# Kernel optimization log

Hardware: AMD Instinct MI355X
Metric: run time of the kernel (lower is better)

The kernel has to match this reference:

```python
import jax, jax.numpy as jnp
import numpy as np
from itertools import product

L0 = (41, 1600, 1408)  # sparse_shape (z,y,x) from pc_range / voxel_size + [1,0,0]
B = 4
N_PER = 25000
PNAMES = ['w_in','s_in','b_in','w1','s1','b1','w2a','s2a','b2a','w2b','s2b','b2b','w2c','s2c','b2c','w3a','s3a','b3a','w3b','s3b','b3b','w3c','s3c','b3c','w4a','s4a','b4a','w4b','s4b','b4b','w4c','s4c','b4c','w_out','s_out','b_out']


def _enc(c, shape):
    D, H, W = shape
    return ((c[:, 0].astype(np.int64) * D + c[:, 1]) * H + c[:, 2]) * W + c[:, 3]


def _subm_rb(coords, shape):
    # submanifold conv rulebook: out site i gathers input j with coord_j = coord_i + offset
    N = coords.shape[0]
    keys = _enc(coords, shape)
    order = np.argsort(keys); sk = keys[order]
    ins, outs = [], []
    for dz, dy, dx in product((-1, 0, 1), repeat=3):
        nb = coords.astype(np.int64).copy()
        nb[:, 1] += dz; nb[:, 2] += dy; nb[:, 3] += dx
        ok = ((nb[:, 1] >= 0) & (nb[:, 1] < shape[0]) & (nb[:, 2] >= 0) & (nb[:, 2] < shape[1]) & (nb[:, 3] >= 0) & (nb[:, 3] < shape[2]))
        qi = np.nonzero(ok)[0]
        qk = _enc(nb[qi], shape)
        pos = np.clip(np.searchsorted(sk, qk), 0, N - 1)
        f = sk[pos] == qk
        ins.append(order[pos[f]].astype(np.int32))
        outs.append(qi[f].astype(np.int32))
    R = max(len(a) for a in ins)
    rin = np.zeros((27, R), np.int32); rout = np.full((27, R), N, np.int32)  # pad -> dummy out row
    for k in range(27):
        rin[k, :len(ins[k])] = ins[k]; rout[k, :len(outs[k])] = outs[k]
    return jnp.asarray(rin), jnp.asarray(rout)


def _spconv_rb(coords, shape, ks, st, pd):
    # strided sparse conv: out = (in + pad - k) / stride where divisible and in-bounds
    osh = tuple((shape[i] + 2 * pd[i] - ks[i]) // st[i] + 1 for i in range(3))
    per = []; allk = []
    for off in product(*[range(k) for k in ks]):
        oc = np.empty((coords.shape[0], 4), np.int64)
        oc[:, 0] = coords[:, 0]
        ok = np.ones(coords.shape[0], bool)
        for d in range(3):
            v = coords[:, d + 1].astype(np.int64) + pd[d] - off[d]
            ok &= (v % st[d] == 0)
            v = v // st[d]
            ok &= (v >= 0) & (v < osh[d])
            oc[:, d + 1] = v
        qi = np.nonzero(ok)[0]
        qk = _enc(oc[qi], osh)
        per.append((qi.astype(np.int32), qk)); allk.append(qk)
    uk = np.unique(np.concatenate(allk))
    Nout = len(uk); K = len(per)
    R = max(len(qi) for qi, _ in per)
    rin = np.zeros((K, R), np.int32); rout = np.full((K, R), Nout, np.int32)
    for k, (qi, qk) in enumerate(per):
        rin[k, :len(qi)] = qi
        rout[k, :len(qi)] = np.searchsorted(uk, qk).astype(np.int32)
    t = uk.copy()
    x = t % osh[2]; t //= osh[2]; y = t % osh[1]; t //= osh[1]; z = t % osh[0]; b = t // osh[0]
    ocoords = np.stack([b, z, y, x], 1).astype(np.int32)
    return jnp.asarray(rin), jnp.asarray(rout), ocoords, osh


def _gen_coords(rng):
    # clustered LiDAR-like voxel occupancy: gaussian clusters so 3x3x3 neighborhoods are populated
    out = []
    for b in range(B):
        nc = 250
        ctr = np.stack([rng.integers(6, 34, nc), rng.integers(60, 1540, nc), rng.integers(60, 1348, nc)], 1)
        pts = ctr[np.repeat(np.arange(nc), 400)] + rng.normal(0.0, 2.0, (nc * 400, 3))
        pts = np.rint(pts).astype(np.int64)
        for d in range(3):
            pts[:, d] = np.clip(pts[:, d], 0, L0[d] - 1)
        keys = (pts[:, 0] * L0[1] + pts[:, 1]) * L0[2] + pts[:, 2]
        _, ui = np.unique(keys, return_index=True)
        assert len(ui) >= N_PER
        c = pts[np.sort(ui[:N_PER])]
        out.append(np.concatenate([np.full((N_PER, 1), b, np.int64), c], 1))
    return np.concatenate(out, 0).astype(np.int32)


def _conv(feat, W, rin, rout, nout):
    # gather -> per-offset GEMM -> scatter-add (spconv rulebook algorithm)
    out = jnp.zeros((nout + 1, W.shape[2]), feat.dtype)  # +1 dummy row for padding
    for k in range(W.shape[0]):
        out = out.at[rout[k]].add(feat[rin[k]] @ W[k])
    return out[:nout]


def _bnrelu(x, s, b):
    # eval-mode BatchNorm1d folded to affine, then ReLU
    return jax.nn.relu(x * s + b)


def _net(voxels, normalizer, rb1_in, rb1_out, rb2s_in, rb2s_out, batch2, rb2_in, rb2_out, rb3s_in, rb3s_out, batch3, rb3_in, rb3_out, rb4s_in, rb4s_out, batch4, rb4_in, rb4_out, rbo_in, rbo_out, batch_out, P):
    n0 = voxels.shape[0]; n2 = batch2.shape[0]; n3 = batch3.shape[0]; n4 = batch4.shape[0]; no = batch_out.shape[0]
    f = voxels.sum(1) / normalizer  # mean VFE: (N0, 4)
    x = _bnrelu(_conv(f, P['w_in'], rb1_in, rb1_out, n0), P['s_in'], P['b_in'])
    x = _bnrelu(_conv(x, P['w1'], rb1_in, rb1_out, n0), P['s1'], P['b1'])
    x = _bnrelu(_conv(x, P['w2a'], rb2s_in, rb2s_out, n2), P['s2a'], P['b2a'])
    x = _bnrelu(_conv(x, P['w2b'], rb2_in, rb2_out, n2), P['s2b'], P['b2b'])
    x = _bnrelu(_conv(x, P['w2c'], rb2_in, rb2_out, n2), P['s2c'], P['b2c'])
    x = _bnrelu(_conv(x, P['w3a'], rb3s_in, rb3s_out, n3), P['s3a'], P['b3a'])
    x = _bnrelu(_conv(x, P['w3b'], rb3_in, rb3_out, n3), P['s3b'], P['b3b'])
    x = _bnrelu(_conv(x, P['w3c'], rb3_in, rb3_out, n3), P['s3c'], P['b3c'])
    x = _bnrelu(_conv(x, P['w4a'], rb4s_in, rb4s_out, n4), P['s4a'], P['b4a'])
    x = _bnrelu(_conv(x, P['w4b'], rb4_in, rb4_out, n4), P['s4b'], P['b4b'])
    x = _bnrelu(_conv(x, P['w4c'], rb4_in, rb4_out, n4), P['s4c'], P['b4c'])
    x = _bnrelu(_conv(x, P['w_out'], rbo_in, rbo_out, no), P['s_out'], P['b_out'])
    # per-batch global max pool over active voxels (== F.max_pool1d over voxel dim)
    return jax.ops.segment_max(x, batch_out.astype(jnp.int32), num_segments=B)


def setup_inputs():
    rng = np.random.default_rng(0)
    coords0 = _gen_coords(rng)
    rb1_in, rb1_out = _subm_rb(coords0, L0)
    rb2s_in, rb2s_out, c2, sh2 = _spconv_rb(coords0, L0, (3, 3, 3), (2, 2, 2), (1, 1, 1))
    rb2_in, rb2_out = _subm_rb(c2, sh2)
    rb3s_in, rb3s_out, c3, sh3 = _spconv_rb(c2, sh2, (3, 3, 3), (2, 2, 2), (1, 1, 1))
    rb3_in, rb3_out = _subm_rb(c3, sh3)
    rb4s_in, rb4s_out, c4, sh4 = _spconv_rb(c3, sh3, (3, 3, 3), (2, 2, 2), (0, 1, 1))
    rb4_in, rb4_out = _subm_rb(c4, sh4)
    rbo_in, rbo_out, co, _ = _spconv_rb(c4, sh4, (3, 1, 1), (2, 1, 1), (0, 0, 0))
    N0 = coords0.shape[0]
    d = dict(
        voxels=jnp.asarray(rng.normal(0, 1, (N0, 5, 4)).astype(np.float32)),
        voxel_num_points=jnp.asarray(rng.integers(1, 6, N0).astype(np.int32)),
        voxel_coords=jnp.asarray(coords0),
        rb1_in=rb1_in, rb1_out=rb1_out,
        rb2s_in=rb2s_in, rb2s_out=rb2s_out, batch2=jnp.asarray(c2[:, 0]),
        rb2_in=rb2_in, rb2_out=rb2_out,
        rb3s_in=rb3s_in, rb3s_out=rb3s_out, batch3=jnp.asarray(c3[:, 0]),
        rb3_in=rb3_in, rb3_out=rb3_out,
        rb4s_in=rb4s_in, rb4s_out=rb4s_out, batch4=jnp.asarray(c4[:, 0]),
        rb4_in=rb4_in, rb4_out=rb4_out,
        rbo_in=rbo_in, rbo_out=rbo_out, batch_out=jnp.asarray(co[:, 0]),
    )
    def _w(k, ci, co_):
        return jnp.asarray((rng.normal(0, 1, (k, ci, co_)) / np.sqrt(k * ci)).astype(np.float32))
    def _bn(c):
        return (jnp.asarray(rng.uniform(0.5, 1.5, c).astype(np.float32)), jnp.asarray(rng.normal(0, 0.1, c).astype(np.float32)))
    d['w_in'] = _w(27, 4, 16); d['s_in'], d['b_in'] = _bn(16)
    d['w1'] = _w(27, 16, 16); d['s1'], d['b1'] = _bn(16)
    d['w2a'] = _w(27, 16, 32); d['s2a'], d['b2a'] = _bn(32)
    d['w2b'] = _w(27, 32, 32); d['s2b'], d['b2b'] = _bn(32)
    d['w2c'] = _w(27, 32, 32); d['s2c'], d['b2c'] = _bn(32)
    d['w3a'] = _w(27, 32, 64); d['s3a'], d['b3a'] = _bn(64)
    d['w3b'] = _w(27, 64, 64); d['s3b'], d['b3b'] = _bn(64)
    d['w3c'] = _w(27, 64, 64); d['s3c'], d['b3c'] = _bn(64)
    d['w4a'] = _w(27, 64, 64); d['s4a'], d['b4a'] = _bn(64)
    d['w4b'] = _w(27, 64, 64); d['s4b'], d['b4b'] = _bn(64)
    d['w4c'] = _w(27, 64, 64); d['s4c'], d['b4c'] = _bn(64)
    d['w_out'] = _w(3, 64, 128); d['s_out'], d['b_out'] = _bn(128)
    return d


def reference(voxels, voxel_num_points, voxel_coords, rb1_in, rb1_out, rb2s_in, rb2s_out, batch2, rb2_in, rb2_out, rb3s_in, rb3s_out, batch3, rb3_in, rb3_out, rb4s_in, rb4s_out, batch4, rb4_in, rb4_out, rbo_in, rbo_out, batch_out, w_in, s_in, b_in, w1, s1, b1, w2a, s2a, b2a, w2b, s2b, b2b, w2c, s2c, b2c, w3a, s3a, b3a, w3b, s3b, b3b, w3c, s3c, b3c, w4a, s4a, b4a, w4b, s4b, b4b, w4c, s4c, b4c, w_out, s_out, b_out):
    normalizer = jnp.maximum(voxel_num_points.astype(voxels.dtype), 1.0)[:, None]
    P = dict(zip(PNAMES, (w_in, s_in, b_in, w1, s1, b1, w2a, s2a, b2a, w2b, s2b, b2b, w2c, s2c, b2c, w3a, s3a, b3a, w3b, s3b, b3b, w3c, s3c, b3c, w4a, s4a, b4a, w4b, s4b, b4b, w4c, s4c, b4c, w_out, s_out, b_out)))
    return _net(voxels, normalizer, rb1_in, rb1_out, rb2s_in, rb2s_out, batch2, rb2_in, rb2_out, rb3s_in, rb3s_out, batch3, rb3_in, rb3_out, rb4s_in, rb4s_out, batch4, rb4_in, rb4_out, rbo_in, rbo_out, batch_out, P)
```

## Files before the change

kernel.cpp:

```cpp
#include <hip/hip_runtime.h>
#include <cstddef>
#include <cstdint>

typedef _Float16 half8 __attribute__((ext_vector_type(8)));
typedef float floatx4 __attribute__((ext_vector_type(4)));
typedef float floatx16 __attribute__((ext_vector_type(16)));

static inline int cdiv_i(int a, int b) { return (a + b - 1) / b; }

struct RB { const int* rin; const int* rout; int K, R, nout, start, end, off; };
struct RBs { RB d[8]; };
__global__ void rb_fill_all(RBs P, int* __restrict__ tbl, int total) {
  int idx = blockIdx.x * blockDim.x + threadIdx.x;
  if (idx >= total) return;
#pragma unroll
  for (int l = 0; l < 8; ++l) {
    if (idx >= P.d[l].start && idx < P.d[l].end) {
      const RB rb = P.d[l];
      int e = idx - rb.start;
      int o = rb.rout[e];
      if ((unsigned)o < (unsigned)rb.nout) {
        int k = e / rb.R;
        tbl[rb.off + (size_t)k * rb.nout + o] = rb.rin[e];
      }
    }
  }
}

__global__ void tbl_fill_kernel(const int* __restrict__ rin,
                                const int* __restrict__ rout,
                                int* __restrict__ tbl, int K, int R, int nout) {
  int e = blockIdx.x * blockDim.x + threadIdx.x;
  if (e >= K * R) return;
  int o = rout[e];
  if ((unsigned)o >= (unsigned)nout) return;
  int k = e / R;
  tbl[(size_t)k * nout + o] = rin[e];
}

struct WP { const float* W; int K, Ci, CiPad, Co, start, end, off, p32; };
struct WPs {
  WP d[12];
  const float* vox; const int* vnp; _Float16* f0; int featTot, N0;
  float* dout; int outTot, wStart, wEnd;
};
__global__ void prep_all(WPs P, _Float16* __restrict__ Bp, int total) {
  int idx = blockIdx.x * blockDim.x + threadIdx.x;
  if (idx >= total) return;
  if (idx < P.featTot) {
    int i = idx >> 3, c = idx & 7;
    float v = 0.f;
    if (i < P.N0 && c < 4) {
      const float* p = P.vox + (size_t)i * 20 + c;
      v = (p[0] + p[4] + p[8] + p[12] + p[16]) / fmaxf((float)P.vnp[i], 1.f);
    }
    P.f0[idx] = (_Float16)v;
    return;
  }
  if (idx < P.featTot + P.outTot) {
    P.dout[idx - P.featTot] = 0.f;
    return;
  }
  int widx = idx - P.featTot - P.outTot;
#pragma unroll
  for (int l = 0; l < 12; ++l) {
    if (widx >= P.d[l].start && widx < P.d[l].end) {
      const WP w = P.d[l];
      int e = widx - w.start;
      int j = e & 7;
      int lane = (e >> 3) & 63;
      int rest = e >> 9;
      float v;
      if (w.p32) {
        int NT = w.Co >> 5;
        int t = rest % NT, ch = rest / NT;
        int SUB = w.CiPad >> 4;
        int ko = ch / SUB, s = ch % SUB;
        int ci = s * 16 + ((lane >> 5) << 3) + j;
        int col = t * 32 + (lane & 31);
        v = w.W[((size_t)ko * w.Ci + ci) * w.Co + col];
      } else {
        int NT = w.Co >> 4;
        int t = rest % NT, ch = rest / NT;
        int kk = ch * 32 + ((lane >> 4) << 3) + j;
        int k = kk / w.CiPad, ci = kk % w.CiPad;
        int n = t * 16 + (lane & 15);
        v = (k < w.K && ci < w.Ci) ? w.W[((size_t)k * w.Ci + ci) * w.Co + n] : 0.f;
      }
      Bp[w.off + e] = (_Float16)v;
    }
  }
}

template <int K, int CiPad, int Co, int KS, int CG, int CBLK>
__global__ __launch_bounds__(256) void conv_mfma(
    const _Float16* __restrict__ feat, const _Float16* __restrict__ Bp,
    const int* __restrict__ tbl, const float* __restrict__ sc,
    const float* __restrict__ bi, _Float16* __restrict__ out,
    int nout, int nin) {
  constexpr int NT = Co / 16;
  constexpr int NTE = NT / CBLK;
  constexpr int NTW = NTE / CG;
  constexpr int RG = 4 / (KS * CG);
  static_assert(KS * CG * RG == 4 && RG >= 1 && NT % CBLK == 0 && NTE % CG == 0);
  constexpr int NCH = (K * CiPad + 31) / 32;
  constexpr int L2C = (CiPad == 8) ? 3 : 4;
  constexpr int DIV = (CiPad >= 32) ? (CiPad / 32) : 1;
  constexpr int CoP = NTE * 16 + 4;

  __shared__ float red[(KS > 1) ? (KS - 1) * RG * 16 * CoP : 1];

  if (blockIdx.x == 0 && threadIdx.x < Co)
    out[(size_t)nout * Co + threadIdx.x] = (_Float16)0.f;

  int id = blockIdx.x;
  { int nb = gridDim.x, nb8 = (nb >> 3) << 3;
    if (id < nb8) { int per = nb >> 3; id = (id & 7) * per + (id >> 3); } }
  const int rt = id / CBLK, cb = id % CBLK;
  const int wave = threadIdx.x >> 6, lane = threadIdx.x & 63;
  const int ks = wave % KS;
  const int cg = (wave / KS) % CG;
  const int rowg = wave / (KS * CG);
  const int m = lane & 15, lb = (lane >> 4) * 8;
  const int i0 = (rt * RG + rowg) * 16;
  if constexpr (KS == 1) { if (i0 >= nout) return; }
  const int row = i0 + m;
  const bool rOK = row < nout;
  const int ct0 = cb * NTE + cg * NTW;

  floatx4 acc[NTW];
#pragma unroll
  for (int n = 0; n < NTW; ++n) { floatx4 z = {0,0,0,0}; acc[n] = z; }

  if constexpr (CiPad >= 32) {
    constexpr int NKW = (K + KS - 1) / KS;
    constexpr int NC = NKW * DIV;
    constexpr int DA = NC < 8 ? NC : 8;
    constexpr int DB = NC < 2 ? NC : 2;
    int idx[NKW];
#pragma unroll
    for (int q = 0; q < NKW; ++q) {
      int k = ks * NKW + q;
      int jj = (rOK && k < K) ? tbl[(size_t)k * nout + row] : -1;
      idx[q] = (jj < 0) ? nin : jj;
    }
    half8 ap[DA]; half8 bq[DB][NTW];
#pragma unroll
    for (int d = 0; d < DA; ++d)
      ap[d] = *(const half8*)(feat + (size_t)idx[d / DIV] * CiPad + (d % DIV) * 32 + lb);
#pragma unroll
    for (int d = 0; d < DB; ++d) {
      int k = ks * NKW + d / DIV;
      int ch = ((k < K) ? k : (K - 1)) * DIV + (d % DIV);
#pragma unroll
      for (int n = 0; n < NTW; ++n)
        bq[d][n] = *(const half8*)(Bp + ((size_t)ch * NT * 64 + lane) * 8 +
                                   (size_t)(ct0 + n) * 512);
    }
#pragma unroll
    for (int ii = 0; ii < NC; ++ii) {
      half8 a = ap[ii % DA];
      half8 bt[NTW];
#pragma unroll
      for (int n = 0; n < NTW; ++n) bt[n] = bq[ii % DB][n];
      if (ii + DA < NC) {
        int nx = ii + DA;
        ap[ii % DA] = *(const half8*)(feat + (size_t)idx[nx / DIV] * CiPad +
                                      (nx % DIV) * 32 + lb);
      }
      if (ii + DB < NC) {
        int nx = ii + DB;
        int k = ks * NKW + nx / DIV;
        int ch = ((k < K) ? k : (K - 1)) * DIV + (nx % DIV);
#pragma unroll
        for (int n = 0; n < NTW; ++n)
          bq[ii % DB][n] = *(const half8*)(Bp + ((size_t)ch * NT * 64 + lane) * 8 +
                                           (size_t)(ct0 + n) * 512);
      }
#pragma unroll
      for (int n = 0; n < NTW; ++n)
        acc[n] = __builtin_amdgcn_mfma_f32_16x16x32_f16(a, bt[n], acc[n], 0, 0, 0);
    }
  } else {
    constexpr int NCW = (NCH + KS - 1) / KS;
    constexpr int DA = NCW < 8 ? NCW : 8;
    constexpr int DB = NCW < 2 ? NCW : 2;
    int idx[NCW];
#pragma unroll
    for (int q = 0; q < NCW; ++q) {
      int ch = ks * NCW + q;
      int ko = (ch * 32 + lb) >> L2C;
      int jj = (rOK && ko < K && ch < NCH) ? tbl[(size_t)ko * nout + row] : -1;
      idx[q] = (jj < 0) ? nin : jj;
    }
    half8 ap[DA]; half8 bq[DB][NTW];
#pragma unroll
    for (int d = 0; d < DA; ++d) {
      int ch = ks * NCW + d;
      ap[d] = *(const half8*)(feat + (size_t)idx[d] * CiPad + ((ch * 32 + lb) & (CiPad - 1)));
    }
#pragma unroll
    for (int d = 0; d < DB; ++d) {
      int ch = ks * NCW + d;
      if (ch >= NCH) ch = NCH - 1;
#pragma unroll
      for (int n = 0; n < NTW; ++n)
        bq[d][n] = *(const half8*)(Bp + ((size_t)ch * NT * 64 + lane) * 8 +
                                   (size_t)(ct0 + n) * 512);
    }
#pragma unroll
    for (int ii = 0; ii < NCW; ++ii) {
      half8 a = ap[ii % DA];
      half8 bt[NTW];
#pragma unroll
      for (int n = 0; n < NTW; ++n) bt[n] = bq[ii % DB][n];
      if (ii + DA < NCW) {
        int nx = ii + DA;
        int ch = ks * NCW + nx;
        ap[ii % DA] = *(const half8*)(feat + (size_t)idx[nx] * CiPad +
                                      ((ch * 32 + lb) & (CiPad - 1)));
      }
      if (ii + DB < NCW) {
        int nx = ii + DB;
        int ch = ks * NCW + nx;
        if (ch >= NCH) ch = NCH - 1;
#pragma unroll
        for (int n = 0; n < NTW; ++n)
          bq[ii % DB][n] = *(const half8*)(Bp + ((size_t)ch * NT * 64 + lane) * 8 +
                                           (size_t)(ct0 + n) * 512);
      }
#pragma unroll
      for (int n = 0; n < NTW; ++n)
        acc[n] = __builtin_amdgcn_mfma_f32_16x16x32_f16(a, bt[n], acc[n], 0, 0, 0);
    }
  }

  const int rl = (lane >> 4) * 4;
  if constexpr (KS > 1) {
    if (ks > 0) {
#pragma unroll
      for (int n = 0; n < NTW; ++n) {
        int lcol = (cg * NTW + n) * 16 + m;
#pragma unroll
        for (int r = 0; r < 4; ++r)
          red[((ks - 1) * RG + rowg) * 16 * CoP + (rl + r) * CoP + lcol] = acc[n][r];
      }
    }
    __syncthreads();
    if (ks > 0) return;
#pragma unroll
    for (int s = 1; s < KS; ++s)
#pragma unroll
      for (int n = 0; n < NTW; ++n) {
        int lcol = (cg * NTW + n) * 16 + m;
#pragma unroll
        for (int r = 0; r < 4; ++r)
          acc[n][r] += red[((s - 1) * RG + rowg) * 16 * CoP + (rl + r) * CoP + lcol];
      }
  }

#pragma unroll
  for (int n = 0; n < NTW; ++n) {
    int col = (ct0 + n) * 16 + m;
    float s_ = sc[col], b_ = bi[col];
#pragma unroll
    for (int r = 0; r < 4; ++r) {
      int orow = i0 + rl + r;
      if (orow < nout)
        out[(size_t)orow * Co + col] = (_Float16)fmaxf(fmaf(acc[n][r], s_, b_), 0.f);
    }
  }
}

template <int K, int CiPad, int Co, int KS, int CG, int CBLK>
__global__ __launch_bounds__(256) void conv_mfma32(
    const _Float16* __restrict__ feat, const _Float16* __restrict__ Bp,
    const int* __restrict__ tbl, const float* __restrict__ sc,
    const float* __restrict__ bi, _Float16* __restrict__ out,
    int nout, int nin) {
  constexpr int NT = Co / 32;
  constexpr int NTE = NT / CBLK;
  constexpr int NTW = NTE / CG;
  constexpr int RG = 4 / (KS * CG);
  static_assert(KS * CG * RG == 4 && RG >= 1 && NT % CBLK == 0 && NTE % CG == 0 && NTW >= 1);
  constexpr int SUB = CiPad / 16;
  constexpr int NKW = (K + KS - 1) / KS;
  constexpr int NC = NKW * SUB;
  constexpr int DA = NC < 8 ? NC : 8;
  constexpr int DB = NC < 2 ? NC : 2;
  constexpr int CoP = NTE * 32 + 4;

  __shared__ float red[(KS > 1) ? (KS - 1) * RG * 32 * CoP : 1];

  if (blockIdx.x == 0 && threadIdx.x < Co)
    out[(size_t)nout * Co + threadIdx.x] = (_Float16)0.f;

  int id = blockIdx.x;
  { int nb = gridDim.x, nb8 = (nb >> 3) << 3;
    if (id < nb8) { int per = nb >> 3; id = (id & 7) * per + (id >> 3); } }
  const int rt = id / CBLK, cb = id % CBLK;
  const int wave = threadIdx.x >> 6, lane = threadIdx.x & 63;
  const int ks = wave % KS;
  const int cg = (wave / KS) % CG;
  const int rowg = wave / (KS * CG);
  const int m = lane & 31, lb = (lane >> 5) * 8, h = lane >> 5;
  const int i0 = (rt * RG + rowg) * 32;
  if constexpr (KS == 1) { if (i0 >= nout) return; }
  const int row = i0 + m;
  const bool rOK = row < nout;
  const int ct0 = cb * NTE + cg * NTW;

  floatx16 acc[NTW];
#pragma unroll
  for (int n = 0; n < NTW; ++n)
#pragma unroll
    for (int r = 0; r < 16; ++r) acc[n][r] = 0.f;

  int idx[NKW];
#pragma unroll
  for (int q = 0; q < NKW; ++q) {
    int k = ks * NKW + q;
    int jj = (rOK && k < K) ? tbl[(size_t)k * nout + row] : -1;
    idx[q] = (jj < 0) ? nin : jj;
  }

  half8 ap[DA]; half8 bq[DB][NTW];
#pragma unroll
  for (int d = 0; d < DA; ++d)
    ap[d] = *(const half8*)(feat + (size_t)idx[d / SUB] * CiPad + (d % SUB) * 16 + lb);
#pragma unroll
  for (int d = 0; d < DB; ++d) {
    int k = ks * NKW + d / SUB;
    int ch = ((k < K) ? k : (K - 1)) * SUB + (d % SUB);
#pragma unroll
    for (int n = 0; n < NTW; ++n)
      bq[d][n] = *(const half8*)(Bp + (size_t)(ch * NT + ct0 + n) * 512 + lane * 8);
  }
#pragma unroll
  for (int ii = 0; ii < NC; ++ii) {
    half8 a = ap[ii % DA];
    half8 bt[NTW];
#pragma unroll
    for (int n = 0; n < NTW; ++n) bt[n] = bq[ii % DB][n];
    if (ii + DA < NC) {
      int nx = ii + DA;
      ap[ii % DA] = *(const half8*)(feat + (size_t)idx[nx / SUB] * CiPad +
                                    (nx % SUB) * 16 + lb);
    }
    if (ii + DB < NC) {
      int nx = ii + DB;
      int k = ks * NKW + nx / SUB;
      int ch = ((k < K) ? k : (K - 1)) * SUB + (nx % SUB);
#pragma unroll
      for (int n = 0; n < NTW; ++n)
        bq[ii % DB][n] = *(const half8*)(Bp + (size_t)(ch * NT + ct0 + n) * 512 + lane * 8);
    }
#pragma unroll
    for (int n = 0; n < NTW; ++n)
      acc[n] = __builtin_amdgcn_mfma_f32_32x32x16_f16(a, bt[n], acc[n], 0, 0, 0);
  }

  if constexpr (KS > 1) {
    if (ks > 0) {
#pragma unroll
      for (int n = 0; n < NTW; ++n) {
        int lcol = (cg * NTW + n) * 32 + m;
#pragma unroll
        for (int reg = 0; reg < 16; ++reg) {
          int r = (reg & 3) + 8 * (reg >> 2) + 4 * h;
          red[((ks - 1) * RG + rowg) * 32 * CoP + r * CoP + lcol] = acc[n][reg];
        }
      }
    }
    __syncthreads();
    if (ks > 0) return;
#pragma unroll
    for (int s = 1; s < KS; ++s)
#pragma unroll
      for (int n = 0; n < NTW; ++n) {
        int lcol = (cg * NTW + n) * 32 + m;
#pragma unroll
        for (int reg = 0; reg < 16; ++reg) {
          int r = (reg & 3) + 8 * (reg >> 2) + 4 * h;
          acc[n][reg] += red[((s - 1) * RG + rowg) * 32 * CoP + r * CoP + lcol];
        }
      }
  }

#pragma unroll
  for (int n = 0; n < NTW; ++n) {
    int col = (ct0 + n) * 32 + m;
    float s_ = sc[col], b_ = bi[col];
#pragma unroll
    for (int reg = 0; reg < 16; ++reg) {
      int orow = i0 + (reg & 3) + 8 * (reg >> 2) + 4 * h;
      if (orow < nout)
        out[(size_t)orow * Co + col] = (_Float16)fmaxf(fmaf(acc[n][reg], s_, b_), 0.f);
    }
  }
}

__global__ __launch_bounds__(256) void segmax2(const _Float16* __restrict__ x,
                                               const int* __restrict__ batch,
                                               int n, float* __restrict__ out) {
  const int RPB = 128;
  int c = threadIdx.x & 127, g = threadIdx.x >> 7;
  int r0 = blockIdx.x * RPB + g;
  int rend = min(n, blockIdx.x * RPB + RPB);
  float mx = 0.f;
  int cb = -1;
  for (int r = r0; r < rend; r += 2) {
    int b = batch[r];
    if (b != cb) {
      if (cb >= 0) atomicMax((int*)out + ((size_t)cb << 7) + c, __float_as_int(mx));
      cb = b; mx = 0.f;
    }
    mx = fmaxf(mx, (float)x[(size_t)r * 128 + c]);
  }
  if (cb >= 0) atomicMax((int*)out + ((size_t)cb << 7) + c, __float_as_int(mx));
}

extern "C" void kernel_launch(void* const* d_in, const int* in_sizes, int n_in,
                              void* d_out, int out_size, void* d_ws, size_t ws_size,
                              hipStream_t stream) {
  auto I = [&](int idx) { return (const int*)d_in[idx]; };
  auto F = [&](int idx) { return (const float*)d_in[idx]; };

  const int N0  = in_sizes[1];
  const int R1  = in_sizes[3] / 27;
  const int R2s = in_sizes[5] / 27;
  const int n2  = in_sizes[7];
  const int R2  = in_sizes[8] / 27;
  const int R3s = in_sizes[10] / 27;
  const int n3  = in_sizes[12];
  const int R3  = in_sizes[13] / 27;
  const int R4s = in_sizes[15] / 27;
  const int n4  = in_sizes[17];
  const int R4  = in_sizes[18] / 27;
  const int Ro  = in_sizes[20] / 3;
  const int no  = in_sizes[22];

  const int wIdx[12] = {23, 26, 29, 32, 35, 38, 41, 44, 47, 50, 53, 56};
  const int Ks[12]   = {27, 27, 27, 27, 27, 27, 27, 27, 27, 27, 27, 3};
  const int Cis[12]  = {4, 16, 16, 32, 32, 32, 64, 64, 64, 64, 64, 64};
  const int Cos[12]  = {16, 16, 32, 32, 32, 64, 64, 64, 64, 64, 64, 128};
  const int P32[12]  = {0, 0, 0, 1, 1, 1, 1, 1, 1, 1, 1, 0};
  WPs P;
  int wtot = 0;
  int bpOff[12];
  for (int l = 0; l < 12; ++l) {
    int cip = Cis[l] < 8 ? 8 : Cis[l];
    int sz;
    if (P32[l]) sz = Ks[l] * (cip / 16) * (Cos[l] / 32) * 512;
    else        sz = ((Ks[l] * cip + 31) / 32) * (Cos[l] / 16) * 512;
    P.d[l].W = F(wIdx[l]);
    P.d[l].K = Ks[l]; P.d[l].Ci = Cis[l]; P.d[l].CiPad = cip; P.d[l].Co = Cos[l];
    P.d[l].start = wtot; P.d[l].end = wtot + sz; P.d[l].off = wtot; P.d[l].p32 = P32[l];
    bpOff[l] = wtot;
    wtot += sz;
  }

  RBs RP;
  const int rbRin[8]  = {3, 5, 8, 10, 13, 15, 18, 20};
  const int rbRs[8]   = {R1, R2s, R2, R3s, R3, R4s, R4, Ro};
  const int rbKs[8]   = {27, 27, 27, 27, 27, 27, 27, 3};
  const int rbNout[8] = {N0, n2, n2, n3, n3, n4, n4, no};
  size_t tblInts[8], tblOff[8];
  size_t totTbl = 0;
  int totFill = 0;
  for (int l = 0; l < 8; ++l) {
    tblInts[l] = (size_t)rbNout[l] * rbKs[l];
    tblOff[l] = totTbl;
    totTbl += tblInts[l];
    RP.d[l].rin = I(rbRin[l]);
    RP.d[l].rout = I(rbRin[l] + 1);
    RP.d[l].K = rbKs[l]; RP.d[l].R = rbRs[l]; RP.d[l].nout = rbNout[l];
    RP.d[l].start = totFill;
    totFill += rbKs[l] * rbRs[l];
    RP.d[l].end = totFill;
    RP.d[l].off = (int)tblOff[l];
  }

  size_t S = (size_t)(N0 + 1) * 16;
  auto smax = [&](size_t v) { if (v > S) S = v; };
  smax((size_t)(n2 + 1) * 32);
  smax((size_t)(n3 + 1) * 64);
  smax((size_t)(n4 + 1) * 64);
  smax((size_t)(no + 1) * 128);
  S = (S + 7) & ~(size_t)7;

  _Float16* h = (_Float16*)d_ws;
  size_t off = 0;
  _Float16* f0 = h + off;   off += (size_t)(N0 + 1) * 8;
  _Float16* bufA = h + off; off += S;
  _Float16* bufB = h + off; off += S;
  _Float16* Bp = h + off;   off += (size_t)((wtot + 7) & ~7);
  int* tblBase = (int*)(h + off);
  size_t usedBytes = off * 2;
  bool prebuilt = (usedBytes + totTbl * 4 <= ws_size);

  P.vox = F(0); P.vnp = I(1); P.f0 = f0;
  P.featTot = (N0 + 1) * 8; P.N0 = N0;
  P.dout = (float*)d_out; P.outTot = out_size;
  int prepTot = P.featTot + P.outTot + wtot;
  prep_all<<<cdiv_i(prepTot, 256), 256, 0, stream>>>(P, Bp, prepTot);

  const int l2rb[12] = {0, 0, 1, 2, 2, 3, 4, 4, 5, 6, 6, 7};
  const int* tblL[12];
  if (prebuilt) {
    hipMemsetAsync(tblBase, 0xFF, totTbl * 4, stream);
    rb_fill_all<<<cdiv_i(totFill, 256), 256, 0, stream>>>(RP, tblBase, totFill);
    for (int l = 0; l < 12; ++l) tblL[l] = tblBase + tblOff[l2rb[l]];
  } else {
    for (int l = 0; l < 12; ++l) tblL[l] = tblBase;
  }
  auto buildSeq = [&](int rb) {
    if (prebuilt) return;
    hipMemsetAsync(tblBase, 0xFF, tblInts[rb] * 4, stream);
    tbl_fill_kernel<<<cdiv_i(rbKs[rb] * rbRs[rb], 256), 256, 0, stream>>>(
        I(rbRin[rb]), I(rbRin[rb] + 1), tblBase, rbKs[rb], rbRs[rb], rbNout[rb]);
  };

#define CONV16(Kk, CIP, CO, KSv, CGv, CBv, IN, LI, OUTB, NOUT, NIN)           \
  do {                                                                        \
    constexpr int rowsPerBlk = (4 / (KSv * CGv)) * 16;                        \
    int nblk = cdiv_i(NOUT, rowsPerBlk) * CBv;                                \
    conv_mfma<Kk, CIP, CO, KSv, CGv, CBv><<<nblk, 256, 0, stream>>>(          \
        IN, Bp + bpOff[LI], tblL[LI], F(wIdx[LI] + 1), F(wIdx[LI] + 2),       \
        OUTB, NOUT, NIN);                                                     \
  } while (0)
#define CONV32(Kk, CIP, CO, KSv, CGv, CBv, IN, LI, OUTB, NOUT, NIN)           \
  do {                                                                        \
    constexpr int rowsPerBlk = (4 / (KSv * CGv)) * 32;                        \
    int nblk = cdiv_i(NOUT, rowsPerBlk) * CBv;                                \
    conv_mfma32<Kk, CIP, CO, KSv, CGv, CBv><<<nblk, 256, 0, stream>>>(        \
        IN, Bp + bpOff[LI], tblL[LI], F(wIdx[LI] + 1), F(wIdx[LI] + 2),       \
        OUTB, NOUT, NIN);                                                     \
  } while (0)

  buildSeq(0);
  CONV16(27, 8, 16, 1, 1, 1, f0, 0, bufA, N0, N0);
  CONV16(27, 16, 16, 2, 1, 1, bufA, 1, bufB, N0, N0);
  buildSeq(1);
  CONV16(27, 16, 32, 2, 1, 1, bufB, 2, bufA, n2, N0);
  buildSeq(2);
  CONV32(27, 32, 32, 4, 1, 1, bufA, 3, bufB, n2, n2);
  CONV32(27, 32, 32, 4, 1, 1, bufB, 4, bufA, n2, n2);
  buildSeq(3);
  CONV32(27, 32, 64, 4, 1, 1, bufA, 5, bufB, n3, n2);
  buildSeq(4);
  CONV32(27, 64, 64, 4, 1, 1, bufB, 6, bufA, n3, n3);
  CONV32(27, 64, 64, 4, 1, 1, bufA, 7, bufB, n3, n3);
  buildSeq(5);
  CONV32(27, 64, 64, 4, 1, 1, bufB, 8, bufA, n4, n3);
  buildSeq(6);
  CONV32(27, 64, 64, 4, 1, 1, bufA, 9, bufB, n4, n4);
  CONV32(27, 64, 64, 4, 1, 1, bufB, 10, bufA, n4, n4);
  buildSeq(7);
  CONV16(3, 64, 128, 2, 2, 2, bufA, 11, bufB, no, n4);
  segmax2<<<cdiv_i(no, 128), 256, 0, stream>>>(bufB, I(22), no, (float*)d_out);
#undef CONV16
#undef CONV32
}
```

Baseline: 433.5 us.

## Fuse segment-max into output conv, fold table memset into prep, split conv columns

The final conv now applies BN/ReLU and atomically max-reduces its results per batch directly into the output, which removes the intermediate fp16 buffer write and the separate segmax kernel. The rulebook table -1 initialisation moves from a hipMemset into the prep kernel, saving one launch. The 64-channel mfma32 convs now split output columns across two blocks (CBLK=2), which raises parallelism but gathers the input rows twice. The fused epilogue issues one atomic per element instead of one per segment run, so atomic contention on the small output rises.

```diff
diff --git a/kernel.cpp b/kernel.cpp
--- a/kernel.cpp
+++ b/kernel.cpp
@@ -42,7 +42,8 @@
 struct WPs {
   WP d[12];
   const float* vox; const int* vnp; _Float16* f0; int featTot, N0;
-  float* dout; int outTot, wStart, wEnd;
+  float* dout; int outTot;
+  int* tbl; int tblTot;
 };
 __global__ void prep_all(WPs P, _Float16* __restrict__ Bp, int total) {
   int idx = blockIdx.x * blockDim.x + threadIdx.x;
@@ -57,11 +58,17 @@
     P.f0[idx] = (_Float16)v;
     return;
   }
-  if (idx < P.featTot + P.outTot) {
-    P.dout[idx - P.featTot] = 0.f;
+  idx -= P.featTot;
+  if (idx < P.outTot) {
+    P.dout[idx] = 0.f;
     return;
   }
-  int widx = idx - P.featTot - P.outTot;
+  idx -= P.outTot;
+  if (idx < P.tblTot) {
+    P.tbl[idx] = -1;
+    return;
+  }
+  int widx = idx - P.tblTot;
 #pragma unroll
   for (int l = 0; l < 12; ++l) {
     if (widx >= P.d[l].start && widx < P.d[l].end) {
@@ -92,11 +99,12 @@
   }
 }
 
-template <int K, int CiPad, int Co, int KS, int CG, int CBLK>
+template <int K, int CiPad, int Co, int KS, int CG, int CBLK, bool SMX = false>
 __global__ __launch_bounds__(256) void conv_mfma(
     const _Float16* __restrict__ feat, const _Float16* __restrict__ Bp,
     const int* __restrict__ tbl, const float* __restrict__ sc,
     const float* __restrict__ bi, _Float16* __restrict__ out,
+    const int* __restrict__ batch, float* __restrict__ dst,
     int nout, int nin) {
   constexpr int NT = Co / 16;
   constexpr int NTE = NT / CBLK;
@@ -110,8 +118,10 @@
 
   __shared__ float red[(KS > 1) ? (KS - 1) * RG * 16 * CoP : 1];
 
-  if (blockIdx.x == 0 && threadIdx.x < Co)
-    out[(size_t)nout * Co + threadIdx.x] = (_Float16)0.f;
+  if constexpr (!SMX) {
+    if (blockIdx.x == 0 && threadIdx.x < Co)
+      out[(size_t)nout * Co + threadIdx.x] = (_Float16)0.f;
+  }
 
   int id = blockIdx.x;
   { int nb = gridDim.x, nb8 = (nb >> 3) << 3;
@@ -266,8 +276,15 @@
 #pragma unroll
     for (int r = 0; r < 4; ++r) {
       int orow = i0 + rl + r;
-      if (orow < nout)
-        out[(size_t)orow * Co + col] = (_Float16)fmaxf(fmaf(acc[n][r], s_, b_), 0.f);
+      if (orow < nout) {
+        float v = fmaxf(fmaf(acc[n][r], s_, b_), 0.f);
+        if constexpr (SMX) {
+          int b = batch[orow];
+          atomicMax((int*)dst + (size_t)b * Co + col, __float_as_int(v));
+        } else {
+          out[(size_t)orow * Co + col] = (_Float16)v;
+        }
+      }
     }
   }
 }
@@ -398,26 +415,6 @@
         out[(size_t)orow * Co + col] = (_Float16)fmaxf(fmaf(acc[n][reg], s_, b_), 0.f);
     }
   }
-}
-
-__global__ __launch_bounds__(256) void segmax2(const _Float16* __restrict__ x,
-                                               const int* __restrict__ batch,
-                                               int n, float* __restrict__ out) {
-  const int RPB = 128;
-  int c = threadIdx.x & 127, g = threadIdx.x >> 7;
-  int r0 = blockIdx.x * RPB + g;
-  int rend = min(n, blockIdx.x * RPB + RPB);
-  float mx = 0.f;
-  int cb = -1;
-  for (int r = r0; r < rend; r += 2) {
-    int b = batch[r];
-    if (b != cb) {
-      if (cb >= 0) atomicMax((int*)out + ((size_t)cb << 7) + c, __float_as_int(mx));
-      cb = b; mx = 0.f;
-    }
-    mx = fmaxf(mx, (float)x[(size_t)r * 128 + c]);
-  }
-  if (cb >= 0) atomicMax((int*)out + ((size_t)cb << 7) + c, __float_as_int(mx));
 }
 
 extern "C" void kernel_launch(void* const* d_in, const int* in_sizes, int n_in,
@@ -502,13 +499,14 @@
   P.vox = F(0); P.vnp = I(1); P.f0 = f0;
   P.featTot = (N0 + 1) * 8; P.N0 = N0;
   P.dout = (float*)d_out; P.outTot = out_size;
-  int prepTot = P.featTot + P.outTot + wtot;
+  if (prebuilt) { P.tbl = tblBase; P.tblTot = (int)totTbl; }
+  else          { P.tbl = nullptr; P.tblTot = 0; }
+  int prepTot = P.featTot + P.outTot + P.tblTot + wtot;
   prep_all<<<cdiv_i(prepTot, 256), 256, 0, stream>>>(P, Bp, prepTot);
 
   const int l2rb[12] = {0, 0, 1, 2, 2, 3, 4, 4, 5, 6, 6, 7};
   const int* tblL[12];
   if (prebuilt) {
-    hipMemsetAsync(tblBase, 0xFF, totTbl * 4, stream);
     rb_fill_all<<<cdiv_i(totFill, 256), 256, 0, stream>>>(RP, tblBase, totFill);
     for (int l = 0; l < 12; ++l) tblL[l] = tblBase + tblOff[l2rb[l]];
   } else {
@@ -527,7 +525,15 @@
     int nblk = cdiv_i(NOUT, rowsPerBlk) * CBv;                                \
     conv_mfma<Kk, CIP, CO, KSv, CGv, CBv><<<nblk, 256, 0, stream>>>(          \
         IN, Bp + bpOff[LI], tblL[LI], F(wIdx[LI] + 1), F(wIdx[LI] + 2),       \
-        OUTB, NOUT, NIN);                                                     \
+        OUTB, nullptr, nullptr, NOUT, NIN);                                   \
+  } while (0)
+#define CONV16S(Kk, CIP, CO, KSv, CGv, CBv, IN, LI, NOUT, NIN)                \
+  do {                                                                        \
+    constexpr int rowsPerBlk = (4 / (KSv * CGv)) * 16;                        \
+    int nblk = cdiv_i(NOUT, rowsPerBlk) * CBv;                                \
+    conv_mfma<Kk, CIP, CO, KSv, CGv, CBv, true><<<nblk, 256, 0, stream>>>(    \
+        IN, Bp + bpOff[LI], tblL[LI], F(wIdx[LI] + 1), F(wIdx[LI] + 2),       \
+        nullptr, I(22), (float*)d_out, NOUT, NIN);                            \
   } while (0)
 #define CONV32(Kk, CIP, CO, KSv, CGv, CBv, IN, LI, OUTB, NOUT, NIN)           \
   do {                                                                        \
@@ -547,18 +553,18 @@
   CONV32(27, 32, 32, 4, 1, 1, bufA, 3, bufB, n2, n2);
   CONV32(27, 32, 32, 4, 1, 1, bufB, 4, bufA, n2, n2);
   buildSeq(3);
-  CONV32(27, 32, 64, 4, 1, 1, bufA, 5, bufB, n3, n2);
+  CONV32(27, 32, 64, 4, 1, 2, bufA, 5, bufB, n3, n2);
   buildSeq(4);
-  CONV32(27, 64, 64, 4, 1, 1, bufB, 6, bufA, n3, n3);
-  CONV32(27, 64, 64, 4, 1, 1, bufA, 7, bufB, n3, n3);
+  CONV32(27, 64, 64, 4, 1, 2, bufB, 6, bufA, n3, n3);
+  CONV32(27, 64, 64, 4, 1, 2, bufA, 7, bufB, n3, n3);
   buildSeq(5);
-  CONV32(27, 64, 64, 4, 1, 1, bufB, 8, bufA, n4, n3);
+  CONV32(27, 64, 64, 4, 1, 2, bufB, 8, bufA, n4, n3);
   buildSeq(6);
-  CONV32(27, 64, 64, 4, 1, 1, bufA, 9, bufB, n4, n4);
-  CONV32(27, 64, 64, 4, 1, 1, bufB, 10, bufA, n4, n4);
+  CONV32(27, 64, 64, 4, 1, 2, bufA, 9, bufB, n4, n4);
+  CONV32(27, 64, 64, 4, 1, 2, bufB, 10, bufA, n4, n4);
   buildSeq(7);
-  CONV16(3, 64, 128, 2, 2, 2, bufA, 11, bufB, no, n4);
-  segmax2<<<cdiv_i(no, 128), 256, 0, stream>>>(bufB, I(22), no, (float*)d_out);
+  CONV16S(3, 64, 128, 2, 2, 2, bufA, 11, no, n4);
 #undef CONV16
+#undef CONV16S
 #undef CONV32
 }
```

Result: slower. 592.5 us (+36.7%).
